# Kernel optimization log

Hardware: AMD Instinct MI355X
Metric: run time of the kernel (lower is better)

The kernel has to match this reference:

```python
import jax, jax.numpy as jnp
import numpy as np

N_NODES = 32768
N_EDGES = 524288
N_FEAT = 256
HID = 256
N_GRAPHS = 64
N_CLASSES = 4
NODES_PER_GRAPH = N_NODES // N_GRAPHS
BN_EPS = 1e-5


def setup_inputs() -> dict:
    key = jax.random.key(0)
    ks = jax.random.split(key, 16)
    x = jax.random.normal(ks[0], (N_NODES, N_FEAT), dtype=jnp.float32)
    edge_index = jax.random.randint(ks[1], (2, N_EDGES), 0, N_NODES, dtype=jnp.int32)
    batch = (jnp.arange(N_NODES, dtype=jnp.int32) // NODES_PER_GRAPH)
    def xavier(k, shape):
        fan_in, fan_out = shape[0], shape[1]
        a = float(np.sqrt(6.0 / (fan_in + fan_out)))
        return jax.random.uniform(k, shape, jnp.float32, -a, a)
    return {
        "x": x, "edge_index": edge_index, "batch": batch,
        "W1": xavier(ks[2], (N_FEAT, HID)), "b1": jnp.zeros((HID,), jnp.float32),
        "g1": jnp.ones((HID,), jnp.float32), "be1": jnp.zeros((HID,), jnp.float32),
        "W2": xavier(ks[3], (HID, HID)), "b2": jnp.zeros((HID,), jnp.float32),
        "g2": jnp.ones((HID,), jnp.float32), "be2": jnp.zeros((HID,), jnp.float32),
        "W_ih": xavier(ks[4], (HID, 4 * HID)), "W_hh": xavier(ks[5], (HID, 4 * HID)),
        "b_ih": jnp.zeros((4 * HID,), jnp.float32), "b_hh": jnp.zeros((4 * HID,), jnp.float32),
        "W_fc": xavier(ks[6], (HID, N_CLASSES)), "b_fc": jnp.zeros((N_CLASSES,), jnp.float32),
    }


def gcn_conv(x, W, b, src, dst):
    # PyG GCNConv: add self-loops, symmetric normalization, aggregate, then bias
    h = x @ W                                   # [N, H]
    deg = jnp.zeros((x.shape[0],), h.dtype).at[dst].add(1.0) + 1.0  # in-deg + self-loop
    dinv = jax.lax.rsqrt(deg)
    coef = dinv[src] * dinv[dst]                # [E]
    msg = h[src] * coef[:, None]                # gather + scale, [E, H]
    agg = jnp.zeros_like(h).at[dst].add(msg)    # scatter-add
    agg = agg + h * (1.0 / deg)[:, None]        # self-loop term (norm = 1/deg)
    return agg + b


def batch_norm(x, gamma, beta):
    mean = jnp.mean(x, axis=0)
    var = jnp.mean(jnp.square(x - mean), axis=0)  # biased, as torch BN training
    return (x - mean) * jax.lax.rsqrt(var + BN_EPS) * gamma + beta


def reference(x, edge_index, batch, W1, b1, g1, be1, W2, b2, g2, be2,
              W_ih, W_hh, b_ih, b_hh, W_fc, b_fc):
    src, dst = edge_index[0], edge_index[1]
    h = jax.nn.relu(batch_norm(gcn_conv(x, W1, b1, src, dst), g1, be1))
    h = jax.nn.relu(batch_norm(gcn_conv(h, W2, b2, src, dst), g2, be2))
    # global mean pool over graphs
    sums = jax.ops.segment_sum(h, batch, num_segments=N_GRAPHS)
    cnts = jax.ops.segment_sum(jnp.ones((h.shape[0],), h.dtype), batch, num_segments=N_GRAPHS)
    pooled = sums / cnts[:, None]               # [G, H]
    # LSTM, seq_len = 1, zero initial state -> single cell step
    h0 = jnp.zeros((N_GRAPHS, HID), h.dtype)
    c0 = jnp.zeros((N_GRAPHS, HID), h.dtype)
    gates = pooled @ W_ih + h0 @ W_hh + b_ih + b_hh  # [G, 4H]
    i, f, g, o = jnp.split(gates, 4, axis=1)
    c1 = jax.nn.sigmoid(f) * c0 + jax.nn.sigmoid(i) * jnp.tanh(g)
    h1 = jax.nn.sigmoid(o) * jnp.tanh(c1)
    logits = h1 @ W_fc + b_fc
    logp = jax.nn.log_softmax(logits, axis=1)
    return (logp, (h1[None], c1[None]))
```

## Files before the change

kernel.cpp:

```cpp
#include <hip/hip_runtime.h>
#include <math.h>

#define N_NODES 32768
#define N_FEAT 256
#define HID 256
#define N_GRAPHS 64
#define NPG 512
#define N_CLASSES 4
#define BN_EPS 1e-5f

typedef __attribute__((ext_vector_type(8))) short bf16x8;
typedef __attribute__((ext_vector_type(4))) float f32x4;

__device__ __forceinline__ ushort f2b(float f) {
    union { float f; uint u; } v; v.f = f;
    uint u = v.u;
    return (ushort)((u + 0x7FFFu + ((u >> 16) & 1u)) >> 16);
}
__device__ __forceinline__ float bflo(uint u) {
    union { uint u; float f; } v; v.u = u << 16;
    return v.f;
}
__device__ __forceinline__ float bfhi(uint u) {
    union { uint u; float f; } v; v.u = u & 0xFFFF0000u;
    return v.f;
}

__global__ void k_count_prep(const int* __restrict__ dst, int* __restrict__ degcnt, int cntB,
                             const float* __restrict__ x, ushort* __restrict__ xb, int xB,
                             const float* __restrict__ W1, const float* __restrict__ W2,
                             ushort* __restrict__ Wt1, ushort* __restrict__ Wt2,
                             uint* __restrict__ csrs, int E) {
    int b = blockIdx.x;
    int t = threadIdx.x;
    if (b < cntB) {
        int e = b * 256 + t;
        if (e < E) atomicAdd(&degcnt[dst[e]], 1);
    } else if (b < cntB + xB) {
        int i = (b - cntB) * 256 + t;
        float4 v0 = *(const float4*)(x + (size_t)i * 8);
        float4 v1 = *(const float4*)(x + (size_t)i * 8 + 4);
        uint4 o;
        o.x = (uint)f2b(v0.x) | ((uint)f2b(v0.y) << 16);
        o.y = (uint)f2b(v0.z) | ((uint)f2b(v0.w) << 16);
        o.z = (uint)f2b(v1.x) | ((uint)f2b(v1.y) << 16);
        o.w = (uint)f2b(v1.z) | ((uint)f2b(v1.w) << 16);
        *(uint4*)(xb + (size_t)i * 8) = o;
    } else if (b < cntB + xB + 512) {
        int wb = b - cntB - xB;
        const float* W = (wb < 256) ? W1 : W2;
        ushort* Wt = (wb < 256) ? Wt1 : Wt2;
        int n = wb & 255;
        Wt[n * 256 + t] = f2b(W[t * 256 + n]);
    } else {
        int i = (b - cntB - xB - 512) * 256 + t;
        uint4 s = make_uint4(N_NODES, N_NODES, N_NODES, N_NODES);
        *(uint4*)(csrs + (size_t)i * 4) = s;
    }
}

__global__ __launch_bounds__(256) void k_scan1(const int* __restrict__ degcnt,
                                               int* __restrict__ blocksum) {
    int n = blockIdx.x * 256 + threadIdx.x;
    int p = (degcnt[n] + 2) & ~1;
#pragma unroll
    for (int off = 1; off < 64; off <<= 1) p += __shfl_xor(p, off);
    __shared__ int ws[4];
    int lane = threadIdx.x & 63, w = threadIdx.x >> 6;
    if (lane == 0) ws[w] = p;
    __syncthreads();
    if (threadIdx.x == 0)
        blocksum[blockIdx.x] = ws[0] + ws[1] + ws[2] + ws[3];
}

__global__ __launch_bounds__(128) void k_scan2(const int* __restrict__ blocksum,
                                               int* __restrict__ blockoff,
                                               int* __restrict__ row_start,
                                               ushort* __restrict__ hs_pad) {
    int t = threadIdx.x;
    int v = blocksum[t];
    int lane = t & 63, w = t >> 6;
    int inc = v;
#pragma unroll
    for (int off = 1; off < 64; off <<= 1) {
        int u = __shfl_up(inc, off);
        if (lane >= off) inc += u;
    }
    __shared__ int w0tot;
    if (t == 63) w0tot = inc;
    __syncthreads();
    if (w == 1) inc += w0tot;
    blockoff[t] = inc - v;
    if (t == 127) row_start[N_NODES] = inc;
    ((uint*)hs_pad)[t] = 0;
}

__global__ __launch_bounds__(256) void k_scan3(const int* __restrict__ degcnt,
                                               const int* __restrict__ blockoff,
                                               float* __restrict__ dinv,
                                               int* __restrict__ row_start,
                                               int* __restrict__ cursor,
                                               uint* __restrict__ csrs) {
    int t = threadIdx.x;
    int n = blockIdx.x * 256 + t;
    int c = degcnt[n];
    int p = (c + 2) & ~1;
    int lane = t & 63, w = t >> 6;
    int inc = p;
#pragma unroll
    for (int off = 1; off < 64; off <<= 1) {
        int u = __shfl_up(inc, off);
        if (lane >= off) inc += u;
    }
    __shared__ int ws[4];
    if (lane == 63) ws[w] = inc;
    __syncthreads();
    int wadd = 0;
    for (int i = 0; i < w; ++i) wadd += ws[i];
    int run = blockoff[blockIdx.x] + wadd + inc - p;
    row_start[n] = run;
    csrs[run] = (uint)n;
    cursor[n] = run + 1;
    dinv[n] = rsqrtf((float)(c + 1));
}

__global__ void k_fill(const int* __restrict__ src, const int* __restrict__ dst,
                       int* __restrict__ cursor, uint* __restrict__ csrs, int E) {
    int e = blockIdx.x * 256 + threadIdx.x;
    if (e >= E) return;
    int d = dst[e];
    int pos = atomicAdd(&cursor[d], 1);
    csrs[pos] = (uint)src[e];
}

__global__ __launch_bounds__(256) void k_gemm_bf16(const ushort* __restrict__ A,
                                                   const ushort* __restrict__ Bt,
                                                   const float* __restrict__ dinv,
                                                   ushort* __restrict__ hs) {
    __shared__ ushort Bs[128 * 256];
    int tid = threadIdx.x;
    int n0 = blockIdx.x * 128;
    int m0 = blockIdx.y * 128;

#pragma unroll
    for (int c = 0; c < 16; ++c) {
        int g = c * 256 + tid;
        int idx = g * 8;
        int row = idx >> 8;
        int col = idx & 255;
        uint4 v = *(const uint4*)(Bt + (size_t)(n0 + row) * 256 + col);
        int sidx = idx ^ ((row & 7) << 3);
        *(uint4*)(Bs + sidx) = v;
    }
    __syncthreads();

    int wid = tid >> 6;
    int lane = tid & 63;
    int wr = wid >> 1, wc = wid & 1;
    int r = lane & 15;
    int ko = (lane >> 4) * 8;

    const ushort* Ab = A + (size_t)(m0 + wr * 64 + r) * 256 + ko;

    f32x4 acc[4][4] = {};
#pragma unroll
    for (int ks = 0; ks < 8; ++ks) {
        bf16x8 a[4], b[4];
#pragma unroll
        for (int i = 0; i < 4; ++i)
            a[i] = *(const bf16x8*)(Ab + i * (16 * 256) + ks * 32);
#pragma unroll
        for (int j = 0; j < 4; ++j) {
            int srow = wc * 64 + j * 16 + r;
            int idx = (srow * 256 + ko + ks * 32) ^ ((srow & 7) << 3);
            b[j] = *(const bf16x8*)(Bs + idx);
        }
#pragma unroll
        for (int i = 0; i < 4; ++i)
#pragma unroll
            for (int j = 0; j < 4; ++j)
                acc[i][j] = __builtin_amdgcn_mfma_f32_16x16x32_bf16(a[i], b[j], acc[i][j], 0, 0, 0);
    }

    int rr = (lane >> 4) * 4;
    int cc = lane & 15;
#pragma unroll
    for (int i = 0; i < 4; ++i) {
        int row = m0 + wr * 64 + i * 16 + rr;
#pragma unroll
        for (int r2 = 0; r2 < 4; ++r2) {
            float dv = dinv[row + r2];
#pragma unroll
            for (int j = 0; j < 4; ++j) {
                int col = n0 + wc * 64 + j * 16 + cc;
                hs[(size_t)(row + r2) * 256 + col] = f2b(acc[i][j][r2] * dv);
            }
        }
    }
}

__global__ __launch_bounds__(256) void k_agg(const ushort* __restrict__ hs,
                                             const uint* __restrict__ csrs,
                                             const int* __restrict__ row_start,
                                             const float* __restrict__ dinv,
                                             const float* __restrict__ bias,
                                             ushort* __restrict__ aggb) {
    int wid = threadIdx.x >> 6;
    int lane = threadIdx.x & 63;
    int half = lane >> 5;
    int fq = lane & 31;
    int n = blockIdx.x * 4 + wid;

    float dv = dinv[n];
    int base = row_start[n];
    int pairs = (row_start[n + 1] - base) >> 1;

    float a0 = 0.f, a1 = 0.f, a2 = 0.f, a3 = 0.f, a4 = 0.f, a5 = 0.f, a6 = 0.f, a7 = 0.f;

    int t = 0;
    for (; t + 4 <= pairs; t += 4) {
        uint s0 = csrs[base + 2 * t + 0 + half];
        uint s1 = csrs[base + 2 * t + 2 + half];
        uint s2 = csrs[base + 2 * t + 4 + half];
        uint s3 = csrs[base + 2 * t + 6 + half];
        uint4 h0 = *(const uint4*)(hs + (size_t)s0 * 256 + fq * 8);
        uint4 h1 = *(const uint4*)(hs + (size_t)s1 * 256 + fq * 8);
        uint4 h2 = *(const uint4*)(hs + (size_t)s2 * 256 + fq * 8);
        uint4 h3 = *(const uint4*)(hs + (size_t)s3 * 256 + fq * 8);
        a0 += bflo(h0.x) + bflo(h1.x) + bflo(h2.x) + bflo(h3.x);
        a1 += bfhi(h0.x) + bfhi(h1.x) + bfhi(h2.x) + bfhi(h3.x);
        a2 += bflo(h0.y) + bflo(h1.y) + bflo(h2.y) + bflo(h3.y);
        a3 += bfhi(h0.y) + bfhi(h1.y) + bfhi(h2.y) + bfhi(h3.y);
        a4 += bflo(h0.z) + bflo(h1.z) + bflo(h2.z) + bflo(h3.z);
        a5 += bfhi(h0.z) + bfhi(h1.z) + bfhi(h2.z) + bfhi(h3.z);
        a6 += bflo(h0.w) + bflo(h1.w) + bflo(h2.w) + bflo(h3.w);
        a7 += bfhi(h0.w) + bfhi(h1.w) + bfhi(h2.w) + bfhi(h3.w);
    }
    for (; t < pairs; ++t) {
        uint s0 = csrs[base + 2 * t + half];
        uint4 h0 = *(const uint4*)(hs + (size_t)s0 * 256 + fq * 8);
        a0 += bflo(h0.x); a1 += bfhi(h0.x);
        a2 += bflo(h0.y); a3 += bfhi(h0.y);
        a4 += bflo(h0.z); a5 += bfhi(h0.z);
        a6 += bflo(h0.w); a7 += bfhi(h0.w);
    }

    a0 += __shfl_xor(a0, 32); a1 += __shfl_xor(a1, 32);
    a2 += __shfl_xor(a2, 32); a3 += __shfl_xor(a3, 32);
    a4 += __shfl_xor(a4, 32); a5 += __shfl_xor(a5, 32);
    a6 += __shfl_xor(a6, 32); a7 += __shfl_xor(a7, 32);

    if (half == 0) {
        float4 b0 = *(const float4*)&bias[fq * 8];
        float4 b1 = *(const float4*)&bias[fq * 8 + 4];
        float o0 = a0 * dv + b0.x, o1 = a1 * dv + b0.y;
        float o2 = a2 * dv + b0.z, o3 = a3 * dv + b0.w;
        float o4 = a4 * dv + b1.x, o5 = a5 * dv + b1.y;
        float o6 = a6 * dv + b1.z, o7 = a7 * dv + b1.w;
        uint4 ov;
        ov.x = (uint)f2b(o0) | ((uint)f2b(o1) << 16);
        ov.y = (uint)f2b(o2) | ((uint)f2b(o3) << 16);
        ov.z = (uint)f2b(o4) | ((uint)f2b(o5) << 16);
        ov.w = (uint)f2b(o6) | ((uint)f2b(o7) << 16);
        *(uint4*)(aggb + (size_t)n * HID + fq * 8) = ov;
    }
}

__global__ __launch_bounds__(256) void k_bn_stats(const ushort* __restrict__ aggb,
                                                  float* __restrict__ bnsum,
                                                  float* __restrict__ bnsq) {
    int t = threadIdx.x;
    int fq = t & 31;
    int rg = t >> 5;
    int r0 = blockIdx.x * 128 + rg * 16;

    float s[8] = {}, q[8] = {};
    for (int r = 0; r < 16; ++r) {
        uint4 v = *(const uint4*)(aggb + (size_t)(r0 + r) * HID + fq * 8);
        float f0 = bflo(v.x), f1 = bfhi(v.x), f2 = bflo(v.y), f3 = bfhi(v.y);
        float f4 = bflo(v.z), f5 = bfhi(v.z), f6 = bflo(v.w), f7 = bfhi(v.w);
        s[0] += f0; q[0] += f0 * f0;  s[1] += f1; q[1] += f1 * f1;
        s[2] += f2; q[2] += f2 * f2;  s[3] += f3; q[3] += f3 * f3;
        s[4] += f4; q[4] += f4 * f4;  s[5] += f5; q[5] += f5 * f5;
        s[6] += f6; q[6] += f6 * f6;  s[7] += f7; q[7] += f7 * f7;
    }

    __shared__ float red[8][32][16];
#pragma unroll
    for (int i = 0; i < 8; ++i) {
        red[rg][fq][i] = s[i];
        red[rg][fq][8 + i] = q[i];
    }
    __syncthreads();
    int fq2 = t & 31;
    int vg = t >> 5;
#pragma unroll
    for (int k = 0; k < 2; ++k) {
        int v = vg * 2 + k;
        float acc = 0.f;
#pragma unroll
        for (int rgi = 0; rgi < 8; ++rgi) acc += red[rgi][fq2][v];
        float* dstp = (v < 8) ? bnsum : bnsq;
        atomicAdd(&dstp[fq2 * 8 + (v & 7)], acc);
    }
}

__global__ void k_bn_apply_b(const ushort* __restrict__ x, const float* __restrict__ bnsum,
                             const float* __restrict__ bnsq, const float* __restrict__ gamma,
                             const float* __restrict__ beta, ushort* __restrict__ out) {
    int i = blockIdx.x * 256 + threadIdx.x;
    if (i >= N_NODES * HID / 4) return;
    int f = (i & 63) * 4;
    const float invN = 1.0f / (float)N_NODES;
    uint2 v = *(const uint2*)(x + (size_t)i * 4);
    float vv[4] = {bflo(v.x), bfhi(v.x), bflo(v.y), bfhi(v.y)};
    float r[4];
#pragma unroll
    for (int qq = 0; qq < 4; ++qq) {
        float mean = bnsum[f + qq] * invN;
        float var = bnsq[f + qq] * invN - mean * mean;
        float t = (vv[qq] - mean) * rsqrtf(var + BN_EPS) * gamma[f + qq] + beta[f + qq];
        r[qq] = t > 0.0f ? t : 0.0f;
    }
    uint2 o;
    o.x = (uint)f2b(r[0]) | ((uint)f2b(r[1]) << 16);
    o.y = (uint)f2b(r[2]) | ((uint)f2b(r[3]) << 16);
    *(uint2*)(out + (size_t)i * 4) = o;
}

__global__ __launch_bounds__(256) void k_bn_pool(const ushort* __restrict__ aggb,
                                                 const float* __restrict__ bnsum,
                                                 const float* __restrict__ bnsq,
                                                 const float* __restrict__ gamma,
                                                 const float* __restrict__ beta,
                                                 float* __restrict__ pooled) {
    int g = blockIdx.x >> 4;
    int blk = blockIdx.x & 15;
    int f = threadIdx.x;
    const float invN = 1.0f / (float)N_NODES;
    float mean = bnsum[f] * invN;
    float var = bnsq[f] * invN - mean * mean;
    float sc = rsqrtf(var + BN_EPS) * gamma[f];
    float sh = beta[f] - mean * sc;
    int r0 = g * NPG + blk * 32;
    float s = 0.0f;
#pragma unroll 4
    for (int r = 0; r < 32; ++r) {
        float v = bflo((uint)aggb[(size_t)(r0 + r) * HID + f]) * sc + sh;
        s += v > 0.0f ? v : 0.0f;
    }
    atomicAdd(&pooled[g * HID + f], s);
}

__global__ __launch_bounds__(256) void k_head(const float* __restrict__ pooled,
                                              const float* __restrict__ W_ih,
                                              const float* __restrict__ b_ih,
                                              const float* __restrict__ b_hh,
                                              const float* __restrict__ W_fc,
                                              const float* __restrict__ b_fc,
                                              float* __restrict__ out) {
    __shared__ float p[HID];
    __shared__ float lsum[N_CLASSES][256];
    __shared__ float logits[N_CLASSES];
    int g = blockIdx.x, j = threadIdx.x;
    p[j] = pooled[g * HID + j] * (1.0f / (float)NPG);
    __syncthreads();

    float gi = 0.f, gf = 0.f, gg = 0.f, go = 0.f;
#pragma unroll 4
    for (int k = 0; k < HID; ++k) {
        float pk = p[k];
        const float* w = &W_ih[(size_t)k * (4 * HID) + j];
        gi += pk * w[0];
        gf += pk * w[HID];
        gg += pk * w[2 * HID];
        go += pk * w[3 * HID];
    }
    gi += b_ih[j] + b_hh[j];
    gf += b_ih[HID + j] + b_hh[HID + j];
    gg += b_ih[2 * HID + j] + b_hh[2 * HID + j];
    go += b_ih[3 * HID + j] + b_hh[3 * HID + j];
    (void)gf;

    float si = 1.f / (1.f + expf(-gi));
    float so = 1.f / (1.f + expf(-go));
    float c1 = si * tanhf(gg);
    float h1 = so * tanhf(c1);

    out[N_GRAPHS * N_CLASSES + g * HID + j] = h1;
    out[N_GRAPHS * N_CLASSES + N_GRAPHS * HID + g * HID + j] = c1;

#pragma unroll
    for (int c = 0; c < N_CLASSES; ++c)
        lsum[c][j] = h1 * W_fc[j * N_CLASSES + c];
    __syncthreads();
    for (int s = 128; s > 0; s >>= 1) {
        if (j < s) {
#pragma unroll
            for (int c = 0; c < N_CLASSES; ++c)
                lsum[c][j] += lsum[c][j + s];
        }
        __syncthreads();
    }
    if (j < N_CLASSES) logits[j] = lsum[j][0] + b_fc[j];
    __syncthreads();
    if (j < N_CLASSES) {
        float m = fmaxf(fmaxf(logits[0], logits[1]), fmaxf(logits[2], logits[3]));
        float lse = m + logf(expf(logits[0] - m) + expf(logits[1] - m) +
                             expf(logits[2] - m) + expf(logits[3] - m));
        out[g * N_CLASSES + j] = logits[j] - lse;
    }
}

extern "C" void kernel_launch(void* const* d_in, const int* in_sizes, int n_in,
                              void* d_out, int out_size, void* d_ws, size_t ws_size,
                              hipStream_t stream) {
    const float* x    = (const float*)d_in[0];
    const int*   ei   = (const int*)d_in[1];
    const float* W1   = (const float*)d_in[3];
    const float* b1   = (const float*)d_in[4];
    const float* g1   = (const float*)d_in[5];
    const float* be1  = (const float*)d_in[6];
    const float* W2   = (const float*)d_in[7];
    const float* b2   = (const float*)d_in[8];
    const float* g2   = (const float*)d_in[9];
    const float* be2  = (const float*)d_in[10];
    const float* W_ih = (const float*)d_in[11];
    const float* b_ih = (const float*)d_in[13];
    const float* b_hh = (const float*)d_in[14];
    const float* W_fc = (const float*)d_in[15];
    const float* b_fc = (const float*)d_in[16];
    float* out = (float*)d_out;

    int E = in_sizes[1] / 2;
    const int* src = ei;
    const int* dst = ei + E;

    const size_t MAT = (size_t)N_NODES * HID;
    size_t SZ = ((size_t)E + 2 * N_NODES + 1023) & ~(size_t)1023;

    ushort* aggb = (ushort*)d_ws;
    ushort* xb   = aggb + MAT;
    ushort* hs   = xb + MAT;
    ushort* Wt1  = hs + MAT + 256;
    ushort* Wt2  = Wt1 + 65536;
    float*  dinv = (float*)(Wt2 + 65536);
    int*    row_start = (int*)(dinv + N_NODES);
    int*    cursor    = row_start + N_NODES + 2;
    uint*   csrs      = (uint*)(cursor + N_NODES);
    int*    blocksum  = (int*)(csrs + SZ);
    int*    blockoff  = blocksum + 128;
    int*    degcnt = blockoff + 128;
    float*  bn1sum = (float*)(degcnt + N_NODES);
    float*  bn1sq  = bn1sum + HID;
    float*  bn2sum = bn1sq + HID;
    float*  bn2sq  = bn2sum + HID;
    float*  pooled = bn2sq + HID;
    size_t zeroBytes = (size_t)N_NODES * 4 + 4 * HID * 4 + (size_t)N_GRAPHS * HID * 4;

    dim3 blk(256);
    int edgeBlocks = (E + 255) / 256;
    int n8blk = (int)(MAT / 8 / 256);
    int sentB = (int)(SZ / 1024);
    int vec4Blocks = (int)(MAT / 4 / 256);
    int aggBlocks = N_NODES / 4;
    dim3 gemmGrid(2, N_NODES / 128);

    hipMemsetAsync(degcnt, 0, zeroBytes, stream);

    k_count_prep<<<edgeBlocks + n8blk + 512 + sentB, blk, 0, stream>>>(
        dst, degcnt, edgeBlocks, x, xb, n8blk, W1, W2, Wt1, Wt2, csrs, E);
    k_scan1<<<N_NODES / 256, blk, 0, stream>>>(degcnt, blocksum);
    k_scan2<<<1, dim3(128), 0, stream>>>(blocksum, blockoff, row_start, hs + MAT);
    k_scan3<<<N_NODES / 256, blk, 0, stream>>>(degcnt, blockoff, dinv, row_start, cursor, csrs);
    k_fill<<<edgeBlocks, blk, 0, stream>>>(src, dst, cursor, csrs, E);

    k_gemm_bf16<<<gemmGrid, blk, 0, stream>>>(xb, Wt1, dinv, hs);
    k_agg<<<aggBlocks, blk, 0, stream>>>(hs, csrs, row_start, dinv, b1, aggb);
    k_bn_stats<<<N_NODES / 128, blk, 0, stream>>>(aggb, bn1sum, bn1sq);
    k_bn_apply_b<<<vec4Blocks, blk, 0, stream>>>(aggb, bn1sum, bn1sq, g1, be1, xb);

    k_gemm_bf16<<<gemmGrid, blk, 0, stream>>>(xb, Wt2, dinv, hs);
    k_agg<<<aggBlocks, blk, 0, stream>>>(hs, csrs, row_start, dinv, b2, aggb);
    k_bn_stats<<<N_NODES / 128, blk, 0, stream>>>(aggb, bn2sum, bn2sq);
    k_bn_pool<<<N_GRAPHS * 16, blk, 0, stream>>>(aggb, bn2sum, bn2sq, g2, be2, pooled);

    k_head<<<N_GRAPHS, blk, 0, stream>>>(pooled, W_ih, b_ih, b_hh, W_fc, b_fc, out);
}
```

Measured before the change: 286.6 us.

## Fuse BN1 apply into second GEMM, merge pooling into head, unroll aggregation

The first batch-norm plus ReLU is now applied while the A tiles are loaded in a templated GEMM, so the standalone normalise pass and its full-matrix write and read are gone. The second BN, pooling and LSTM head are merged into one kernel with 64 blocks, which also drops the pooled buffer and its zeroing. The neighbour-gather loop in aggregation is unrolled to 8 pairs, with 2-pair and 1-pair tails, for more loads in flight. The merged pool kernel runs one block per graph over 512 rows, giving far less parallelism than the previous 1024-block pooling pass and risking a latency-bound tail.

```diff
diff --git a/kernel.cpp b/kernel.cpp
--- a/kernel.cpp
+++ b/kernel.cpp
@@ -133,14 +133,28 @@
     csrs[pos] = (uint)src[e];
 }
 
-__global__ __launch_bounds__(256) void k_gemm_bf16(const ushort* __restrict__ A,
-                                                   const ushort* __restrict__ Bt,
-                                                   const float* __restrict__ dinv,
-                                                   ushort* __restrict__ hs) {
+template <bool BN_A>
+__device__ __forceinline__ void gemm_body(const ushort* __restrict__ A,
+                                          const ushort* __restrict__ Bt,
+                                          const float* __restrict__ dinv,
+                                          const float* __restrict__ bnsum,
+                                          const float* __restrict__ bnsq,
+                                          const float* __restrict__ gamma,
+                                          const float* __restrict__ beta,
+                                          ushort* __restrict__ hs) {
     __shared__ ushort Bs[128 * 256];
+    __shared__ float2 bnc[256];
     int tid = threadIdx.x;
     int n0 = blockIdx.x * 128;
     int m0 = blockIdx.y * 128;
+
+    if (BN_A) {
+        const float invN = 1.0f / (float)N_NODES;
+        float mean = bnsum[tid] * invN;
+        float var = bnsq[tid] * invN - mean * mean;
+        float sc = rsqrtf(var + BN_EPS) * gamma[tid];
+        bnc[tid] = make_float2(sc, beta[tid] - mean * sc);
+    }
 
 #pragma unroll
     for (int c = 0; c < 16; ++c) {
@@ -166,9 +180,33 @@
 #pragma unroll
     for (int ks = 0; ks < 8; ++ks) {
         bf16x8 a[4], b[4];
-#pragma unroll
-        for (int i = 0; i < 4; ++i)
-            a[i] = *(const bf16x8*)(Ab + i * (16 * 256) + ks * 32);
+        if (BN_A) {
+            int kb = ko + ks * 32;
+            float2 c0 = bnc[kb + 0], c1 = bnc[kb + 1], c2 = bnc[kb + 2], c3 = bnc[kb + 3];
+            float2 c4 = bnc[kb + 4], c5 = bnc[kb + 5], c6 = bnc[kb + 6], c7 = bnc[kb + 7];
+#pragma unroll
+            for (int i = 0; i < 4; ++i) {
+                uint4 v = *(const uint4*)(Ab + i * (16 * 256) + ks * 32);
+                float f0 = fmaxf(bflo(v.x) * c0.x + c0.y, 0.f);
+                float f1 = fmaxf(bfhi(v.x) * c1.x + c1.y, 0.f);
+                float f2 = fmaxf(bflo(v.y) * c2.x + c2.y, 0.f);
+                float f3 = fmaxf(bfhi(v.y) * c3.x + c3.y, 0.f);
+                float f4 = fmaxf(bflo(v.z) * c4.x + c4.y, 0.f);
+                float f5 = fmaxf(bfhi(v.z) * c5.x + c5.y, 0.f);
+                float f6 = fmaxf(bflo(v.w) * c6.x + c6.y, 0.f);
+                float f7 = fmaxf(bfhi(v.w) * c7.x + c7.y, 0.f);
+                uint4 o;
+                o.x = (uint)f2b(f0) | ((uint)f2b(f1) << 16);
+                o.y = (uint)f2b(f2) | ((uint)f2b(f3) << 16);
+                o.z = (uint)f2b(f4) | ((uint)f2b(f5) << 16);
+                o.w = (uint)f2b(f6) | ((uint)f2b(f7) << 16);
+                a[i] = *(bf16x8*)&o;
+            }
+        } else {
+#pragma unroll
+            for (int i = 0; i < 4; ++i)
+                a[i] = *(const bf16x8*)(Ab + i * (16 * 256) + ks * 32);
+        }
 #pragma unroll
         for (int j = 0; j < 4; ++j) {
             int srow = wc * 64 + j * 16 + r;
@@ -197,6 +235,24 @@
             }
         }
     }
+}
+
+__global__ __launch_bounds__(256) void k_gemm_bf16(const ushort* __restrict__ A,
+                                                   const ushort* __restrict__ Bt,
+                                                   const float* __restrict__ dinv,
+                                                   ushort* __restrict__ hs) {
+    gemm_body<false>(A, Bt, dinv, nullptr, nullptr, nullptr, nullptr, hs);
+}
+
+__global__ __launch_bounds__(256) void k_gemm_bn(const ushort* __restrict__ A,
+                                                 const ushort* __restrict__ Bt,
+                                                 const float* __restrict__ dinv,
+                                                 const float* __restrict__ bnsum,
+                                                 const float* __restrict__ bnsq,
+                                                 const float* __restrict__ gamma,
+                                                 const float* __restrict__ beta,
+                                                 ushort* __restrict__ hs) {
+    gemm_body<true>(A, Bt, dinv, bnsum, bnsq, gamma, beta, hs);
 }
 
 __global__ __launch_bounds__(256) void k_agg(const ushort* __restrict__ hs,
@@ -218,25 +274,55 @@
     float a0 = 0.f, a1 = 0.f, a2 = 0.f, a3 = 0.f, a4 = 0.f, a5 = 0.f, a6 = 0.f, a7 = 0.f;
 
     int t = 0;
-    for (; t + 4 <= pairs; t += 4) {
+    for (; t + 8 <= pairs; t += 8) {
         uint s0 = csrs[base + 2 * t + 0 + half];
         uint s1 = csrs[base + 2 * t + 2 + half];
         uint s2 = csrs[base + 2 * t + 4 + half];
         uint s3 = csrs[base + 2 * t + 6 + half];
+        uint s4 = csrs[base + 2 * t + 8 + half];
+        uint s5 = csrs[base + 2 * t + 10 + half];
+        uint s6 = csrs[base + 2 * t + 12 + half];
+        uint s7 = csrs[base + 2 * t + 14 + half];
         uint4 h0 = *(const uint4*)(hs + (size_t)s0 * 256 + fq * 8);
         uint4 h1 = *(const uint4*)(hs + (size_t)s1 * 256 + fq * 8);
         uint4 h2 = *(const uint4*)(hs + (size_t)s2 * 256 + fq * 8);
         uint4 h3 = *(const uint4*)(hs + (size_t)s3 * 256 + fq * 8);
-        a0 += bflo(h0.x) + bflo(h1.x) + bflo(h2.x) + bflo(h3.x);
-        a1 += bfhi(h0.x) + bfhi(h1.x) + bfhi(h2.x) + bfhi(h3.x);
-        a2 += bflo(h0.y) + bflo(h1.y) + bflo(h2.y) + bflo(h3.y);
-        a3 += bfhi(h0.y) + bfhi(h1.y) + bfhi(h2.y) + bfhi(h3.y);
-        a4 += bflo(h0.z) + bflo(h1.z) + bflo(h2.z) + bflo(h3.z);
-        a5 += bfhi(h0.z) + bfhi(h1.z) + bfhi(h2.z) + bfhi(h3.z);
-        a6 += bflo(h0.w) + bflo(h1.w) + bflo(h2.w) + bflo(h3.w);
-        a7 += bfhi(h0.w) + bfhi(h1.w) + bfhi(h2.w) + bfhi(h3.w);
-    }
-    for (; t < pairs; ++t) {
+        uint4 h4 = *(const uint4*)(hs + (size_t)s4 * 256 + fq * 8);
+        uint4 h5 = *(const uint4*)(hs + (size_t)s5 * 256 + fq * 8);
+        uint4 h6 = *(const uint4*)(hs + (size_t)s6 * 256 + fq * 8);
+        uint4 h7 = *(const uint4*)(hs + (size_t)s7 * 256 + fq * 8);
+        a0 += bflo(h0.x) + bflo(h1.x) + bflo(h2.x) + bflo(h3.x)
+            + bflo(h4.x) + bflo(h5.x) + bflo(h6.x) + bflo(h7.x);
+        a1 += bfhi(h0.x) + bfhi(h1.x) + bfhi(h2.x) + bfhi(h3.x)
+            + bfhi(h4.x) + bfhi(h5.x) + bfhi(h6.x) + bfhi(h7.x);
+        a2 += bflo(h0.y) + bflo(h1.y) + bflo(h2.y) + bflo(h3.y)
+            + bflo(h4.y) + bflo(h5.y) + bflo(h6.y) + bflo(h7.y);
+        a3 += bfhi(h0.y) + bfhi(h1.y) + bfhi(h2.y) + bfhi(h3.y)
+            + bfhi(h4.y) + bfhi(h5.y) + bfhi(h6.y) + bfhi(h7.y);
+        a4 += bflo(h0.z) + bflo(h1.z) + bflo(h2.z) + bflo(h3.z)
+            + bflo(h4.z) + bflo(h5.z) + bflo(h6.z) + bflo(h7.z);
+        a5 += bfhi(h0.z) + bfhi(h1.z) + bfhi(h2.z) + bfhi(h3.z)
+            + bfhi(h4.z) + bfhi(h5.z) + bfhi(h6.z) + bfhi(h7.z);
+        a6 += bflo(h0.w) + bflo(h1.w) + bflo(h2.w) + bflo(h3.w)
+            + bflo(h4.w) + bflo(h5.w) + bflo(h6.w) + bflo(h7.w);
+        a7 += bfhi(h0.w) + bfhi(h1.w) + bfhi(h2.w) + bfhi(h3.w)
+            + bfhi(h4.w) + bfhi(h5.w) + bfhi(h6.w) + bfhi(h7.w);
+    }
+    for (; t + 2 <= pairs; t += 2) {
+        uint s0 = csrs[base + 2 * t + 0 + half];
+        uint s1 = csrs[base + 2 * t + 2 + half];
+        uint4 h0 = *(const uint4*)(hs + (size_t)s0 * 256 + fq * 8);
+        uint4 h1 = *(const uint4*)(hs + (size_t)s1 * 256 + fq * 8);
+        a0 += bflo(h0.x) + bflo(h1.x);
+        a1 += bfhi(h0.x) + bfhi(h1.x);
+        a2 += bflo(h0.y) + bflo(h1.y);
+        a3 += bfhi(h0.y) + bfhi(h1.y);
+        a4 += bflo(h0.z) + bflo(h1.z);
+        a5 += bfhi(h0.z) + bfhi(h1.z);
+        a6 += bflo(h0.w) + bflo(h1.w);
+        a7 += bfhi(h0.w) + bfhi(h1.w);
+    }
+    if (t < pairs) {
         uint s0 = csrs[base + 2 * t + half];
         uint4 h0 = *(const uint4*)(hs + (size_t)s0 * 256 + fq * 8);
         a0 += bflo(h0.x); a1 += bfhi(h0.x);
@@ -305,65 +391,35 @@
     }
 }
 
-__global__ void k_bn_apply_b(const ushort* __restrict__ x, const float* __restrict__ bnsum,
-                             const float* __restrict__ bnsq, const float* __restrict__ gamma,
-                             const float* __restrict__ beta, ushort* __restrict__ out) {
-    int i = blockIdx.x * 256 + threadIdx.x;
-    if (i >= N_NODES * HID / 4) return;
-    int f = (i & 63) * 4;
-    const float invN = 1.0f / (float)N_NODES;
-    uint2 v = *(const uint2*)(x + (size_t)i * 4);
-    float vv[4] = {bflo(v.x), bfhi(v.x), bflo(v.y), bfhi(v.y)};
-    float r[4];
-#pragma unroll
-    for (int qq = 0; qq < 4; ++qq) {
-        float mean = bnsum[f + qq] * invN;
-        float var = bnsq[f + qq] * invN - mean * mean;
-        float t = (vv[qq] - mean) * rsqrtf(var + BN_EPS) * gamma[f + qq] + beta[f + qq];
-        r[qq] = t > 0.0f ? t : 0.0f;
-    }
-    uint2 o;
-    o.x = (uint)f2b(r[0]) | ((uint)f2b(r[1]) << 16);
-    o.y = (uint)f2b(r[2]) | ((uint)f2b(r[3]) << 16);
-    *(uint2*)(out + (size_t)i * 4) = o;
-}
-
-__global__ __launch_bounds__(256) void k_bn_pool(const ushort* __restrict__ aggb,
-                                                 const float* __restrict__ bnsum,
-                                                 const float* __restrict__ bnsq,
-                                                 const float* __restrict__ gamma,
-                                                 const float* __restrict__ beta,
-                                                 float* __restrict__ pooled) {
-    int g = blockIdx.x >> 4;
-    int blk = blockIdx.x & 15;
-    int f = threadIdx.x;
-    const float invN = 1.0f / (float)N_NODES;
-    float mean = bnsum[f] * invN;
-    float var = bnsq[f] * invN - mean * mean;
-    float sc = rsqrtf(var + BN_EPS) * gamma[f];
-    float sh = beta[f] - mean * sc;
-    int r0 = g * NPG + blk * 32;
-    float s = 0.0f;
-#pragma unroll 4
-    for (int r = 0; r < 32; ++r) {
-        float v = bflo((uint)aggb[(size_t)(r0 + r) * HID + f]) * sc + sh;
-        s += v > 0.0f ? v : 0.0f;
-    }
-    atomicAdd(&pooled[g * HID + f], s);
-}
-
-__global__ __launch_bounds__(256) void k_head(const float* __restrict__ pooled,
-                                              const float* __restrict__ W_ih,
-                                              const float* __restrict__ b_ih,
-                                              const float* __restrict__ b_hh,
-                                              const float* __restrict__ W_fc,
-                                              const float* __restrict__ b_fc,
-                                              float* __restrict__ out) {
+__global__ __launch_bounds__(256) void k_pool_head(const ushort* __restrict__ aggb,
+                                                   const float* __restrict__ bnsum,
+                                                   const float* __restrict__ bnsq,
+                                                   const float* __restrict__ gamma,
+                                                   const float* __restrict__ beta,
+                                                   const float* __restrict__ W_ih,
+                                                   const float* __restrict__ b_ih,
+                                                   const float* __restrict__ b_hh,
+                                                   const float* __restrict__ W_fc,
+                                                   const float* __restrict__ b_fc,
+                                                   float* __restrict__ out) {
     __shared__ float p[HID];
     __shared__ float lsum[N_CLASSES][256];
     __shared__ float logits[N_CLASSES];
     int g = blockIdx.x, j = threadIdx.x;
-    p[j] = pooled[g * HID + j] * (1.0f / (float)NPG);
+
+    const float invN = 1.0f / (float)N_NODES;
+    float mean = bnsum[j] * invN;
+    float var = bnsq[j] * invN - mean * mean;
+    float sc = rsqrtf(var + BN_EPS) * gamma[j];
+    float sh = beta[j] - mean * sc;
+    float s = 0.0f;
+    int r0 = g * NPG;
+#pragma unroll 8
+    for (int r = 0; r < NPG; ++r) {
+        float v = bflo((uint)aggb[(size_t)(r0 + r) * HID + j]) * sc + sh;
+        s += v > 0.0f ? v : 0.0f;
+    }
+    p[j] = s * (1.0f / (float)NPG);
     __syncthreads();
 
     float gi = 0.f, gf = 0.f, gg = 0.f, go = 0.f;
@@ -394,11 +450,11 @@
     for (int c = 0; c < N_CLASSES; ++c)
         lsum[c][j] = h1 * W_fc[j * N_CLASSES + c];
     __syncthreads();
-    for (int s = 128; s > 0; s >>= 1) {
-        if (j < s) {
+    for (int st = 128; st > 0; st >>= 1) {
+        if (j < st) {
 #pragma unroll
             for (int c = 0; c < N_CLASSES; ++c)
-                lsum[c][j] += lsum[c][j + s];
+                lsum[c][j] += lsum[c][j + st];
         }
         __syncthreads();
     }
@@ -455,14 +511,12 @@
     float*  bn1sq  = bn1sum + HID;
     float*  bn2sum = bn1sq + HID;
     float*  bn2sq  = bn2sum + HID;
-    float*  pooled = bn2sq + HID;
-    size_t zeroBytes = (size_t)N_NODES * 4 + 4 * HID * 4 + (size_t)N_GRAPHS * HID * 4;
+    size_t zeroBytes = (size_t)N_NODES * 4 + 4 * HID * 4;
 
     dim3 blk(256);
     int edgeBlocks = (E + 255) / 256;
     int n8blk = (int)(MAT / 8 / 256);
     int sentB = (int)(SZ / 1024);
-    int vec4Blocks = (int)(MAT / 4 / 256);
     int aggBlocks = N_NODES / 4;
     dim3 gemmGrid(2, N_NODES / 128);
 
@@ -478,12 +532,11 @@
     k_gemm_bf16<<<gemmGrid, blk, 0, stream>>>(xb, Wt1, dinv, hs);
     k_agg<<<aggBlocks, blk, 0, stream>>>(hs, csrs, row_start, dinv, b1, aggb);
     k_bn_stats<<<N_NODES / 128, blk, 0, stream>>>(aggb, bn1sum, bn1sq);
-    k_bn_apply_b<<<vec4Blocks, blk, 0, stream>>>(aggb, bn1sum, bn1sq, g1, be1, xb);
-
-    k_gemm_bf16<<<gemmGrid, blk, 0, stream>>>(xb, Wt2, dinv, hs);
+
+    k_gemm_bn<<<gemmGrid, blk, 0, stream>>>(aggb, Wt2, dinv, bn1sum, bn1sq, g1, be1, hs);
     k_agg<<<aggBlocks, blk, 0, stream>>>(hs, csrs, row_start, dinv, b2, aggb);
     k_bn_stats<<<N_NODES / 128, blk, 0, stream>>>(aggb, bn2sum, bn2sq);
-    k_bn_pool<<<N_GRAPHS * 16, blk, 0, stream>>>(aggb, bn2sum, bn2sq, g2, be2, pooled);
-
-    k_head<<<N_GRAPHS, blk, 0, stream>>>(pooled, W_ih, b_ih, b_hh, W_fc, b_fc, out);
-}
+
+    k_pool_head<<<N_GRAPHS, blk, 0, stream>>>(aggb, bn2sum, bn2sq, g2, be2,
+                                              W_ih, b_ih, b_hh, W_fc, b_fc, out);
+}
```

Result: slower. 295.4 us (+3.0%).
